# Optimization experiments

Hardware: AMD Instinct MI355X
Metric: run time of the kernel (lower is better)

Reference implementation:

```python
import jax, jax.numpy as jnp
import numpy as np

N, F, HD, E, K, T, IDX = 50000, 128, 256, 800000, 3, 7, 0


def setup_inputs() -> dict:
    key = jax.random.key(0)
    ks = jax.random.split(key, 18)
    s = 0.05  # param init scale
    return {
        "x": jax.random.normal(ks[0], (N, F), jnp.float32),
        "edge_index": jax.random.randint(ks[1], (2, E), 0, N),
        "edge_weight": jax.random.uniform(ks[2], (E,), jnp.float32),
        "h": jax.random.normal(ks[3], (N, HD), jnp.float32),
        "c": jax.random.normal(ks[4], (N, HD), jnp.float32),
        # 4 ChebConvs on X and 4 on H (gates i, f, c, o), each with K Chebyshev weights
        "theta_x": jax.random.normal(ks[5], (4, K, F, HD), jnp.float32) * s,
        "bias_x": jnp.zeros((4, HD), jnp.float32),
        "theta_h": jax.random.normal(ks[6], (4, K, HD, HD), jnp.float32) * s,
        "bias_h": jnp.zeros((4, HD), jnp.float32),
        "w_c": jax.random.normal(ks[7], (3, HD), jnp.float32) * s,  # peephole w_c_i, w_c_f, w_c_o
        "b_gate": jnp.zeros((4, HD), jnp.float32),  # b_i, b_f, b_c, b_o
        # decoder LSTM (input_size=1, hidden=HD), torch gate order i, f, g, o
        "w_ih": jax.random.normal(ks[8], (4 * HD, 1), jnp.float32) * s,
        "w_hh": jax.random.normal(ks[9], (4 * HD, HD), jnp.float32) * s,
        "b_ih": jnp.zeros((4 * HD,), jnp.float32),
        "b_hh": jnp.zeros((4 * HD,), jnp.float32),
        "w_out": jax.random.normal(ks[10], (1, HD), jnp.float32) * s,
        "b_out": jnp.zeros((1,), jnp.float32),
    }


def _cheb_stack(feat, src, dst, w_norm):
    """Stacked Chebyshev bases [K, N, d]; L_hat = -A_norm (sym norm, lambda_max=2)."""
    def lhat(v):
        msg = w_norm[:, None] * v[src]              # [E, d] gather
        return -jax.ops.segment_sum(msg, dst, num_segments=N)  # scatter-add
    Tx = [feat]
    if K > 1:
        Tx.append(lhat(feat))
    for _ in range(2, K):
        Tx.append(2.0 * lhat(Tx[-1]) - Tx[-2])
    return jnp.stack(Tx)


def reference(x, edge_index, edge_weight, h, c, theta_x, bias_x, theta_h, bias_h,
              w_c, b_gate, w_ih, w_hh, b_ih, b_hh, w_out, b_out):
    src, dst = edge_index[0], edge_index[1]
    # ChebConv.__norm__: remove self loops, sym-normalized Laplacian, scale by 2/lambda_max=1,
    # add -I -> L_hat off-diag = -w_norm, diag = 0
    w = jnp.where(src == dst, 0.0, edge_weight)
    deg = jax.ops.segment_sum(w, src, num_segments=N)
    dis = jnp.where(deg > 0, jax.lax.rsqrt(jnp.maximum(deg, 1e-20)), 0.0)
    w_norm = dis[src] * w * dis[dst]

    # GConvLSTM encode: one conv per gate on X and on H; bases shared across gates
    gx = jnp.einsum('knf,gkfo->gno', _cheb_stack(x, src, dst, w_norm), theta_x) + bias_x[:, None, :]
    gh = jnp.einsum('knf,gkfo->gno', _cheb_stack(h, src, dst, w_norm), theta_h) + bias_h[:, None, :]
    g = gx + gh  # [4, N, HD] gates i, f, c, o
    I = jax.nn.sigmoid(g[0] + w_c[0] * c + b_gate[0])
    Fg = jax.nn.sigmoid(g[1] + w_c[1] * c + b_gate[1])
    Cn = Fg * c + I * jnp.tanh(g[2] + b_gate[2])
    O = jax.nn.sigmoid(g[3] + w_c[2] * Cn + b_gate[3])
    Hn = O * jnp.tanh(Cn)

    h0 = Hn[IDX:IDX + 1]          # [1, HD]
    c0 = Cn[IDX:IDX + 1]
    inp0 = x[IDX, -1:][None]      # [1, 1]

    def step(carry, _):
        hd, cd, inp = carry
        gates = inp @ w_ih.T + hd @ w_hh.T + b_ih + b_hh  # [1, 4*HD]
        i, f, gg, o = jnp.split(gates, 4, axis=1)
        cn = jax.nn.sigmoid(f) * cd + jax.nn.sigmoid(i) * jnp.tanh(gg)
        hn = jax.nn.sigmoid(o) * jnp.tanh(cn)
        out = hn @ w_out.T + b_out                         # [1, 1]
        return (hn, cn, out), out

    _, outs = jax.lax.scan(step, (h0, c0, inp0), None, length=T)  # [T, 1, 1]
    prediction = outs[:, :, 0]  # squeeze dim 2 -> [T, 1]
    return prediction
```

## Files before the change

### kernel.cpp

```cpp
#include <hip/hip_runtime.h>
#include <math.h>

#define NN 50000
#define FD 128
#define HDIM 256
#define NE 800000
#define NBR_CAP 512
#define M_CAP 8192
#define TT 7
#define TPB 256
#define GB 96
#define PSLICE 12
#define GRP 21
#define SB 32
#define SPIN_CAP 50000000

#define O_NBRCNT   0
#define O_MCNT     64
#define O_HSYNC    128
#define O_DEG      16512
#define O_BITMAP   216512
#define O_ZERO_END 222784
#define O_NBRNODE  222784
#define O_NBRW     224832
#define O_MS       226880
#define O_MD       259648
#define O_MW       292416
#define O_CF1      325184
#define O_CF2      357952
#define O_GPART    390720

__device__ __forceinline__ float sigm(float v) { return 1.f / (1.f + expf(-v)); }
__device__ __forceinline__ float dis_of(float dg) {
    return dg > 0.f ? rsqrtf(fmaxf(dg, 1e-20f)) : 0.f;
}

__global__ void k_nbr(const int* __restrict__ ei, const float* __restrict__ ew,
                      char* __restrict__ ws) {
    int*   nbrCnt = (int*)(ws + O_NBRCNT);
    int*   nbrNode= (int*)(ws + O_NBRNODE);
    float* nbrW   = (float*)(ws + O_NBRW);

    int gid = blockIdx.x * blockDim.x + threadIdx.x;
    if (gid < (O_ZERO_END - O_MCNT) / 4) ((unsigned*)(ws + O_MCNT))[gid] = 0u;

    int e0 = gid * 4;
    if (e0 >= NE) return;
    int4 d4 = *(const int4*)&ei[NE + e0];
    float4 w4 = *(const float4*)&ew[e0];
    int dd[4] = {d4.x, d4.y, d4.z, d4.w};
    float wv[4] = {w4.x, w4.y, w4.z, w4.w};
    #pragma unroll
    for (int k = 0; k < 4; ++k) {
        if (dd[k] == 0 && wv[k] != 0.f) {
            int s = ei[e0 + k];
            if (s != 0) {
                int slot = atomicAdd(nbrCnt, 1);
                if (slot < NBR_CAP) { nbrNode[slot] = s; nbrW[slot] = wv[k]; }
            }
        }
    }
}

__global__ void k_match(const int* __restrict__ ei, const float* __restrict__ ew,
                        char* __restrict__ ws) {
    const int* nbrCnt = (const int*)(ws + O_NBRCNT);
    const int* nbrNode= (const int*)(ws + O_NBRNODE);
    int*      mCnt   = (int*)(ws + O_MCNT);
    int*      mS     = (int*)(ws + O_MS);
    int*      mD     = (int*)(ws + O_MD);
    float*    mW     = (float*)(ws + O_MW);
    unsigned* bitmap = (unsigned*)(ws + O_BITMAP);

    __shared__ int sNode[NBR_CAP];
    __shared__ int sCnt;
    if (threadIdx.x == 0) sCnt = min(*nbrCnt, NBR_CAP);
    __syncthreads();
    int cnt = sCnt;
    for (int i = threadIdx.x; i < cnt; i += blockDim.x) sNode[i] = nbrNode[i];
    __syncthreads();
    if (blockIdx.x == 0 && threadIdx.x == 0) atomicOr(&bitmap[0], 1u);

    int i = blockIdx.x * blockDim.x + threadIdx.x;
    int e0 = i * 4;
    if (e0 >= NE) return;
    int4 s4 = *(const int4*)&ei[e0];
    int4 d4 = *(const int4*)&ei[NE + e0];
    float4 w4 = *(const float4*)&ew[e0];
    int ss[4] = {s4.x, s4.y, s4.z, s4.w};
    int dd[4] = {d4.x, d4.y, d4.z, d4.w};
    float wv[4] = {w4.x, w4.y, w4.z, w4.w};
    bool m[4];
    #pragma unroll
    for (int k = 0; k < 4; ++k) m[k] = (dd[k] == 0);
    for (int j = 0; j < cnt; ++j) {
        int nv = sNode[j];
        #pragma unroll
        for (int k = 0; k < 4; ++k) m[k] |= (dd[k] == nv);
    }
    #pragma unroll
    for (int k = 0; k < 4; ++k) {
        int s = ss[k], d = dd[k];
        float w = wv[k];
        if (s == d || w == 0.f || !m[k]) continue;
        int slot = atomicAdd(mCnt, 1);
        if (slot < M_CAP) { mS[slot] = s; mD[slot] = d; mW[slot] = w; }
        atomicOr(&bitmap[s >> 5], 1u << (s & 31));
        atomicOr(&bitmap[d >> 5], 1u << (d & 31));
    }
}

__global__ void k_deg(const int* __restrict__ ei, const float* __restrict__ ew,
                      char* __restrict__ ws) {
    const unsigned* bitmap = (const unsigned*)(ws + O_BITMAP);
    float* deg = (float*)(ws + O_DEG);
    int i = blockIdx.x * blockDim.x + threadIdx.x;
    int e0 = i * 4;
    if (e0 >= NE) return;
    int4 s4 = *(const int4*)&ei[e0];
    int4 d4 = *(const int4*)&ei[NE + e0];
    float4 w4 = *(const float4*)&ew[e0];
    int ss[4] = {s4.x, s4.y, s4.z, s4.w};
    int dd[4] = {d4.x, d4.y, d4.z, d4.w};
    float wv[4] = {w4.x, w4.y, w4.z, w4.w};
    #pragma unroll
    for (int k = 0; k < 4; ++k) {
        int s = ss[k];
        if (s == dd[k] || wv[k] == 0.f) continue;
        if (bitmap[s >> 5] & (1u << (s & 31)))
            atomicAdd(&deg[s], wv[k]);
    }
}

__global__ void k_coef(char* __restrict__ ws) {
    const float* deg    = (const float*)(ws + O_DEG);
    const int*   nbrCnt = (const int*)(ws + O_NBRCNT);
    const int*   mCnt   = (const int*)(ws + O_MCNT);
    const int*   nbrNode= (const int*)(ws + O_NBRNODE);
    const float* nbrW   = (const float*)(ws + O_NBRW);
    const int*   mS     = (const int*)(ws + O_MS);
    const int*   mD     = (const int*)(ws + O_MD);
    const float* mW     = (const float*)(ws + O_MW);
    float*       cf1    = (float*)(ws + O_CF1);
    float*       cf2    = (float*)(ws + O_CF2);

    __shared__ int sNode[NBR_CAP];
    __shared__ float sWl[NBR_CAP];
    __shared__ int sCnt, sMcnt;
    const int tid = threadIdx.x;
    if (tid == 0) { sCnt = min(*nbrCnt, NBR_CAP); sMcnt = min(*mCnt, M_CAP); }
    __syncthreads();
    const int ncnt = sCnt, mcnt = sMcnt;
    for (int i = tid; i < ncnt; i += TPB) { sNode[i] = nbrNode[i]; sWl[i] = nbrW[i]; }
    __syncthreads();
    const float dis0 = dis_of(deg[0]);
    for (int i = tid; i < mcnt; i += TPB) {
        int sI = mS[i], dI = mD[i];
        float w = mW[i];
        float disd = dis_of(deg[dI]);
        float wn = dis_of(deg[sI]) * w * disd;
        float Wd = 0.f;
        for (int j = 0; j < ncnt; ++j) Wd += (sNode[j] == dI) ? sWl[j] : 0.f;
        cf1[i] = (dI == 0) ? wn : 0.f;
        cf2[i] = wn * (dis0 * disd * Wd);
    }
}

__global__ __launch_bounds__(TPB) void k_graph(
    const float* __restrict__ x, const float* __restrict__ h,
    const float* __restrict__ theta_x, const float* __restrict__ theta_h,
    char* __restrict__ ws) {

    const int*   mCnt = (const int*)(ws + O_MCNT);
    const int*   mS   = (const int*)(ws + O_MS);
    const float* cf1  = (const float*)(ws + O_CF1);
    const float* cf2  = (const float*)(ws + O_CF2);
    float*       gpart= (float*)(ws + O_GPART);

    __shared__ float tp1[GRP][PSLICE], tp2[GRP][PSLICE];
    __shared__ float tslice[PSLICE];
    __shared__ int   sMcnt;

    const int tid = threadIdx.x, bid = blockIdx.x;
    if (tid == 0) sMcnt = min(*mCnt, M_CAP);
    __syncthreads();
    const int mcnt = sMcnt;

    const bool isx = bid < 32;
    const int qstart = bid * PSLICE - (isx ? 0 : 3 * FD);
    const float* fb0 = isx ? x : h;
    const int fstride = isx ? FD : HDIM;

    const int pl = tid % PSLICE, gr = tid / PSLICE;
    const float* fbase = fb0 + (qstart + pl) % fstride;

    float a1 = 0.f, a2 = 0.f;
    if (gr < GRP) {
        int i = gr;
        for (; i + 3 * GRP < mcnt; i += 4 * GRP) {
            int s0 = mS[i], s1 = mS[i + GRP], s2 = mS[i + 2 * GRP], s3 = mS[i + 3 * GRP];
            float c10 = cf1[i], c11 = cf1[i + GRP], c12 = cf1[i + 2 * GRP], c13 = cf1[i + 3 * GRP];
            float c20 = cf2[i], c21 = cf2[i + GRP], c22 = cf2[i + 2 * GRP], c23 = cf2[i + 3 * GRP];
            float v0 = fbase[(size_t)s0 * fstride];
            float v1 = fbase[(size_t)s1 * fstride];
            float v2 = fbase[(size_t)s2 * fstride];
            float v3 = fbase[(size_t)s3 * fstride];
            a1 += c10 * v0 + c11 * v1 + c12 * v2 + c13 * v3;
            a2 += c20 * v0 + c21 * v1 + c22 * v2 + c23 * v3;
        }
        for (; i < mcnt; i += GRP) {
            float v = fbase[(size_t)mS[i] * fstride];
            a1 += cf1[i] * v;
            a2 += cf2[i] * v;
        }
        tp1[gr][pl] = a1; tp2[gr][pl] = a2;
    }
    __syncthreads();
    if (tid < PSLICE) {
        float A1 = 0.f, A2 = 0.f;
        #pragma unroll
        for (int g2 = 0; g2 < GRP; ++g2) { A1 += tp1[g2][tid]; A2 += tp2[g2][tid]; }
        int q = qstart + tid;
        int ko = q / fstride;
        float ff0 = fb0[q % fstride];
        tslice[tid] = (ko == 0) ? ff0 : ((ko == 1) ? -A1 : 2.f * A2 - ff0);
    }
    __syncthreads();

    {
        const float* tb = isx ? theta_x : theta_h;
        const size_t gs = isx ? (size_t)(3 * FD) * HDIM : (size_t)(3 * HDIM) * HDIM;
        float g0 = 0.f, g1 = 0.f, g2v = 0.f, g3 = 0.f;
        #pragma unroll
        for (int pp = 0; pp < PSLICE; ++pp) {
            float tv = tslice[pp];
            const float* row = tb + (size_t)(qstart + pp) * HDIM;
            g0  += tv * row[tid];
            g1  += tv * row[gs + tid];
            g2v += tv * row[2 * gs + tid];
            g3  += tv * row[3 * gs + tid];
        }
        float* gp = gpart + (size_t)bid * 1024;
        gp[tid] = g0;
        gp[HDIM + tid] = g1;
        gp[2 * HDIM + tid] = g2v;
        gp[3 * HDIM + tid] = g3;
    }
}

__global__ __launch_bounds__(TPB) void k_tail2(
    const float* __restrict__ x, const float* __restrict__ c,
    const float* __restrict__ bias_x, const float* __restrict__ bias_h,
    const float* __restrict__ w_c, const float* __restrict__ b_gate,
    const float* __restrict__ w_ih, const float* __restrict__ w_hh,
    const float* __restrict__ b_ih, const float* __restrict__ b_hh,
    const float* __restrict__ w_out, const float* __restrict__ b_out,
    float* __restrict__ out, char* __restrict__ ws) {

    unsigned long long* hsync = (unsigned long long*)(ws + O_HSYNC);
    const float* gpart = (const float*)(ws + O_GPART);

    __shared__ __align__(16) float sh[HDIM];
    __shared__ float sdot[32];
    __shared__ float swsum[4];

    const int tid = threadIdx.x, bid = blockIdx.x;

    const int rl = tid >> 3, seg = tid & 7;
    const int grow = (rl >> 3) * HDIM + bid * 8 + (rl & 7);
    float4 wreg[8];
    #pragma unroll
    for (int k = 0; k < 8; ++k)
        wreg[k] = *(const float4*)&w_hh[(size_t)grow * HDIM + seg * 32 + k * 4];
    const float wih_r = w_ih[grow];
    const float br    = b_ih[grow] + b_hh[grow];
    const float bo    = b_out[0];
    const float wout_r = w_out[tid];

    {
        const int d = tid >> 3, j = tid & 7;
        const int g = d >> 3, kk = d & 7, o = bid * 8 + kk;
        float s = 0.f;
        #pragma unroll
        for (int pb = j; pb < GB; pb += 8) s += gpart[(size_t)pb * 1024 + g * HDIM + o];
        s += __shfl_down(s, 4);
        s += __shfl_down(s, 2);
        s += __shfl_down(s, 1);
        if (j == 0) sdot[d] = s;
    }
    __syncthreads();

    float creg = 0.f;
    if (tid < 8) {
        const int o = bid * 8 + tid;
        float g0 = sdot[tid]      + bias_x[o]            + bias_h[o];
        float g1 = sdot[8 + tid]  + bias_x[HDIM + o]     + bias_h[HDIM + o];
        float g2 = sdot[16 + tid] + bias_x[2 * HDIM + o] + bias_h[2 * HDIM + o];
        float g3 = sdot[24 + tid] + bias_x[3 * HDIM + o] + bias_h[3 * HDIM + o];
        float c0 = c[o];
        float I  = sigm(g0 + w_c[o] * c0 + b_gate[o]);
        float Fg = sigm(g1 + w_c[HDIM + o] * c0 + b_gate[HDIM + o]);
        float Cn = Fg * c0 + I * tanhf(g2 + b_gate[2 * HDIM + o]);
        float O  = sigm(g3 + w_c[2 * HDIM + o] * Cn + b_gate[3 * HDIM + o]);
        float h0 = O * tanhf(Cn);
        creg = Cn;
        unsigned long long pk = (1ull << 32) | (unsigned long long)__float_as_uint(h0);
        __hip_atomic_store(&hsync[o], pk, __ATOMIC_RELAXED, __HIP_MEMORY_SCOPE_SYSTEM);
    }
    if (tid < 64) {
        #pragma unroll
        for (int j = 0; j < 4; ++j) {
            unsigned long long v;
            int sp = 0;
            do {
                v = __hip_atomic_load(&hsync[tid * 4 + j],
                                      __ATOMIC_RELAXED, __HIP_MEMORY_SCOPE_SYSTEM);
                if ((unsigned)(v >> 32) == 1u) break;
                __builtin_amdgcn_s_sleep(1);
            } while (++sp < SPIN_CAP);
            sh[tid * 4 + j] = __uint_as_float((unsigned)v);
        }
    }
    __syncthreads();
    float sinp = x[FD - 1];

    for (int t = 0; t < TT; ++t) {
        float acc = 0.f;
        const float* shh = &sh[seg * 32];
        #pragma unroll
        for (int k = 0; k < 8; ++k) {
            float4 hv = *(const float4*)&shh[k * 4];
            acc += hv.x * wreg[k].x + hv.y * wreg[k].y + hv.z * wreg[k].z + hv.w * wreg[k].w;
        }
        acc += __shfl_down(acc, 4);
        acc += __shfl_down(acc, 2);
        acc += __shfl_down(acc, 1);
        if (seg == 0) sdot[rl] = acc + sinp * wih_r + br;
        __syncthreads();
        if (tid < 8) {
            float iv = sdot[tid], fv = sdot[8 + tid], gv = sdot[16 + tid], ov = sdot[24 + tid];
            float cn = sigm(fv) * creg + sigm(iv) * tanhf(gv);
            float hn = sigm(ov) * tanhf(cn);
            creg = cn;
            unsigned long long pk = (((unsigned long long)(t + 2)) << 32)
                                  | (unsigned long long)__float_as_uint(hn);
            __hip_atomic_store(&hsync[(t + 1) * HDIM + bid * 8 + tid], pk,
                               __ATOMIC_RELAXED, __HIP_MEMORY_SCOPE_SYSTEM);
        }
        if (tid < 64) {
            #pragma unroll
            for (int j = 0; j < 4; ++j) {
                unsigned long long v;
                int sp = 0;
                do {
                    v = __hip_atomic_load(&hsync[(t + 1) * HDIM + tid * 4 + j],
                                          __ATOMIC_RELAXED, __HIP_MEMORY_SCOPE_SYSTEM);
                    if ((unsigned)(v >> 32) == (unsigned)(t + 2)) break;
                    __builtin_amdgcn_s_sleep(1);
                } while (++sp < SPIN_CAP);
                sh[tid * 4 + j] = __uint_as_float((unsigned)v);
            }
        }
        __syncthreads();
        float pw = wout_r * sh[tid];
        pw += __shfl_down(pw, 32);
        pw += __shfl_down(pw, 16);
        pw += __shfl_down(pw, 8);
        pw += __shfl_down(pw, 4);
        pw += __shfl_down(pw, 2);
        pw += __shfl_down(pw, 1);
        if ((tid & 63) == 0) swsum[tid >> 6] = pw;
        __syncthreads();
        float sval = swsum[0] + swsum[1] + swsum[2] + swsum[3] + bo;
        sinp = sval;
        if (bid == 0 && tid == 0) out[t] = sval;
    }
}

extern "C" void kernel_launch(void* const* d_in, const int* in_sizes, int n_in,
                              void* d_out, int out_size, void* d_ws, size_t ws_size,
                              hipStream_t stream) {
    const float* x       = (const float*)d_in[0];
    const int*   ei      = (const int*)d_in[1];
    const float* ew      = (const float*)d_in[2];
    const float* h       = (const float*)d_in[3];
    const float* c       = (const float*)d_in[4];
    const float* theta_x = (const float*)d_in[5];
    const float* bias_x  = (const float*)d_in[6];
    const float* theta_h = (const float*)d_in[7];
    const float* bias_h  = (const float*)d_in[8];
    const float* w_c     = (const float*)d_in[9];
    const float* b_gate  = (const float*)d_in[10];
    const float* w_ih    = (const float*)d_in[11];
    const float* w_hh    = (const float*)d_in[12];
    const float* b_ih    = (const float*)d_in[13];
    const float* b_hh    = (const float*)d_in[14];
    const float* w_out   = (const float*)d_in[15];
    const float* b_out   = (const float*)d_in[16];
    char* ws = (char*)d_ws;
    float* out = (float*)d_out;

    hipMemsetAsync(ws, 0, 64, stream);

    int eb4 = (NE / 4 + TPB - 1) / TPB;
    k_nbr<<<eb4, TPB, 0, stream>>>(ei, ew, ws);
    k_match<<<eb4, TPB, 0, stream>>>(ei, ew, ws);
    k_deg<<<eb4, TPB, 0, stream>>>(ei, ew, ws);
    k_coef<<<1, TPB, 0, stream>>>(ws);
    k_graph<<<GB, TPB, 0, stream>>>(x, h, theta_x, theta_h, ws);
    k_tail2<<<SB, TPB, 0, stream>>>(x, c, bias_x, bias_h, w_c, b_gate,
                                    w_ih, w_hh, b_ih, b_hh, w_out, b_out, out, ws);
}
```

Before: 58.51 us.

## Fuse coefficient computation into graph kernel and widen spin-wait polling

Removes the single-block k_coef kernel and recomputes the per-edge Chebyshev coefficients redundantly inside each k_graph block, staging them chunk by chunk in shared memory. This drops one kernel launch and a serial single-block stage, at the cost of every one of the 96 blocks repeating the coefficient work, including the neighbour-scan loop. Separately, in the LSTM tail every thread now polls one hsync entry without s_sleep, instead of 64 threads polling four entries each. The per-step shared-memory barrier before the output reduction is also removed.

```diff
diff --git a/kernel.cpp b/kernel.cpp
--- a/kernel.cpp
+++ b/kernel.cpp
@@ -12,6 +12,7 @@
 #define GB 96
 #define PSLICE 12
 #define GRP 21
+#define ECHUNK 2048
 #define SB 32
 #define SPIN_CAP 50000000
 
@@ -26,9 +27,7 @@
 #define O_MS       226880
 #define O_MD       259648
 #define O_MW       292416
-#define O_CF1      325184
-#define O_CF2      357952
-#define O_GPART    390720
+#define O_GPART    325184
 
 __device__ __forceinline__ float sigm(float v) { return 1.f / (1.f + expf(-v)); }
 __device__ __forceinline__ float dis_of(float dg) {
@@ -132,7 +131,11 @@
     }
 }
 
-__global__ void k_coef(char* __restrict__ ws) {
+__global__ __launch_bounds__(TPB) void k_graph(
+    const float* __restrict__ x, const float* __restrict__ h,
+    const float* __restrict__ theta_x, const float* __restrict__ theta_h,
+    char* __restrict__ ws) {
+
     const float* deg    = (const float*)(ws + O_DEG);
     const int*   nbrCnt = (const int*)(ws + O_NBRCNT);
     const int*   mCnt   = (const int*)(ws + O_MCNT);
@@ -141,50 +144,22 @@
     const int*   mS     = (const int*)(ws + O_MS);
     const int*   mD     = (const int*)(ws + O_MD);
     const float* mW     = (const float*)(ws + O_MW);
-    float*       cf1    = (float*)(ws + O_CF1);
-    float*       cf2    = (float*)(ws + O_CF2);
-
-    __shared__ int sNode[NBR_CAP];
+    float*       gpart  = (float*)(ws + O_GPART);
+
+    __shared__ int   sNode[NBR_CAP];
     __shared__ float sWl[NBR_CAP];
-    __shared__ int sCnt, sMcnt;
-    const int tid = threadIdx.x;
+    __shared__ float cf1[ECHUNK], cf2[ECHUNK];
+    __shared__ int   sS[ECHUNK];
+    __shared__ float tp1[GRP][PSLICE], tp2[GRP][PSLICE];
+    __shared__ float tslice[PSLICE];
+    __shared__ int   sCnt, sMcnt;
+
+    const int tid = threadIdx.x, bid = blockIdx.x;
     if (tid == 0) { sCnt = min(*nbrCnt, NBR_CAP); sMcnt = min(*mCnt, M_CAP); }
     __syncthreads();
     const int ncnt = sCnt, mcnt = sMcnt;
     for (int i = tid; i < ncnt; i += TPB) { sNode[i] = nbrNode[i]; sWl[i] = nbrW[i]; }
     __syncthreads();
-    const float dis0 = dis_of(deg[0]);
-    for (int i = tid; i < mcnt; i += TPB) {
-        int sI = mS[i], dI = mD[i];
-        float w = mW[i];
-        float disd = dis_of(deg[dI]);
-        float wn = dis_of(deg[sI]) * w * disd;
-        float Wd = 0.f;
-        for (int j = 0; j < ncnt; ++j) Wd += (sNode[j] == dI) ? sWl[j] : 0.f;
-        cf1[i] = (dI == 0) ? wn : 0.f;
-        cf2[i] = wn * (dis0 * disd * Wd);
-    }
-}
-
-__global__ __launch_bounds__(TPB) void k_graph(
-    const float* __restrict__ x, const float* __restrict__ h,
-    const float* __restrict__ theta_x, const float* __restrict__ theta_h,
-    char* __restrict__ ws) {
-
-    const int*   mCnt = (const int*)(ws + O_MCNT);
-    const int*   mS   = (const int*)(ws + O_MS);
-    const float* cf1  = (const float*)(ws + O_CF1);
-    const float* cf2  = (const float*)(ws + O_CF2);
-    float*       gpart= (float*)(ws + O_GPART);
-
-    __shared__ float tp1[GRP][PSLICE], tp2[GRP][PSLICE];
-    __shared__ float tslice[PSLICE];
-    __shared__ int   sMcnt;
-
-    const int tid = threadIdx.x, bid = blockIdx.x;
-    if (tid == 0) sMcnt = min(*mCnt, M_CAP);
-    __syncthreads();
-    const int mcnt = sMcnt;
 
     const bool isx = bid < 32;
     const int qstart = bid * PSLICE - (isx ? 0 : 3 * FD);
@@ -193,28 +168,45 @@
 
     const int pl = tid % PSLICE, gr = tid / PSLICE;
     const float* fbase = fb0 + (qstart + pl) % fstride;
+    const float dis0 = dis_of(deg[0]);
 
     float a1 = 0.f, a2 = 0.f;
-    if (gr < GRP) {
-        int i = gr;
-        for (; i + 3 * GRP < mcnt; i += 4 * GRP) {
-            int s0 = mS[i], s1 = mS[i + GRP], s2 = mS[i + 2 * GRP], s3 = mS[i + 3 * GRP];
-            float c10 = cf1[i], c11 = cf1[i + GRP], c12 = cf1[i + 2 * GRP], c13 = cf1[i + 3 * GRP];
-            float c20 = cf2[i], c21 = cf2[i + GRP], c22 = cf2[i + 2 * GRP], c23 = cf2[i + 3 * GRP];
-            float v0 = fbase[(size_t)s0 * fstride];
-            float v1 = fbase[(size_t)s1 * fstride];
-            float v2 = fbase[(size_t)s2 * fstride];
-            float v3 = fbase[(size_t)s3 * fstride];
-            a1 += c10 * v0 + c11 * v1 + c12 * v2 + c13 * v3;
-            a2 += c20 * v0 + c21 * v1 + c22 * v2 + c23 * v3;
-        }
-        for (; i < mcnt; i += GRP) {
-            float v = fbase[(size_t)mS[i] * fstride];
-            a1 += cf1[i] * v;
-            a2 += cf2[i] * v;
-        }
-        tp1[gr][pl] = a1; tp2[gr][pl] = a2;
-    }
+    for (int c0i = 0; c0i < mcnt; c0i += ECHUNK) {
+        int clen = min(ECHUNK, mcnt - c0i);
+        for (int i = tid; i < clen; i += TPB) {
+            int sI = mS[c0i + i], dI = mD[c0i + i];
+            float w = mW[c0i + i];
+            float disd = dis_of(deg[dI]);
+            float wn = dis_of(deg[sI]) * w * disd;
+            float Wd = 0.f;
+            for (int j = 0; j < ncnt; ++j) Wd += (sNode[j] == dI) ? sWl[j] : 0.f;
+            cf1[i] = (dI == 0) ? wn : 0.f;
+            cf2[i] = wn * (dis0 * disd * Wd);
+            sS[i] = sI;
+        }
+        __syncthreads();
+        if (gr < GRP) {
+            int i = gr;
+            for (; i + 3 * GRP < clen; i += 4 * GRP) {
+                int s0 = sS[i], s1 = sS[i + GRP], s2 = sS[i + 2 * GRP], s3 = sS[i + 3 * GRP];
+                float c10 = cf1[i], c11 = cf1[i + GRP], c12 = cf1[i + 2 * GRP], c13 = cf1[i + 3 * GRP];
+                float c20 = cf2[i], c21 = cf2[i + GRP], c22 = cf2[i + 2 * GRP], c23 = cf2[i + 3 * GRP];
+                float v0 = fbase[(size_t)s0 * fstride];
+                float v1 = fbase[(size_t)s1 * fstride];
+                float v2 = fbase[(size_t)s2 * fstride];
+                float v3 = fbase[(size_t)s3 * fstride];
+                a1 += c10 * v0 + c11 * v1 + c12 * v2 + c13 * v3;
+                a2 += c20 * v0 + c21 * v1 + c22 * v2 + c23 * v3;
+            }
+            for (; i < clen; i += GRP) {
+                float v = fbase[(size_t)sS[i] * fstride];
+                a1 += cf1[i] * v;
+                a2 += cf2[i] * v;
+            }
+        }
+        __syncthreads();
+    }
+    if (gr < GRP) { tp1[gr][pl] = a1; tp2[gr][pl] = a2; }
     __syncthreads();
     if (tid < PSLICE) {
         float A1 = 0.f, A2 = 0.f;
@@ -307,19 +299,14 @@
         unsigned long long pk = (1ull << 32) | (unsigned long long)__float_as_uint(h0);
         __hip_atomic_store(&hsync[o], pk, __ATOMIC_RELAXED, __HIP_MEMORY_SCOPE_SYSTEM);
     }
-    if (tid < 64) {
-        #pragma unroll
-        for (int j = 0; j < 4; ++j) {
-            unsigned long long v;
-            int sp = 0;
-            do {
-                v = __hip_atomic_load(&hsync[tid * 4 + j],
-                                      __ATOMIC_RELAXED, __HIP_MEMORY_SCOPE_SYSTEM);
-                if ((unsigned)(v >> 32) == 1u) break;
-                __builtin_amdgcn_s_sleep(1);
-            } while (++sp < SPIN_CAP);
-            sh[tid * 4 + j] = __uint_as_float((unsigned)v);
-        }
+    {
+        unsigned long long v;
+        int sp = 0;
+        do {
+            v = __hip_atomic_load(&hsync[tid], __ATOMIC_RELAXED, __HIP_MEMORY_SCOPE_SYSTEM);
+            if ((unsigned)(v >> 32) == 1u) break;
+        } while (++sp < SPIN_CAP);
+        sh[tid] = __uint_as_float((unsigned)v);
     }
     __syncthreads();
     float sinp = x[FD - 1];
@@ -347,22 +334,19 @@
             __hip_atomic_store(&hsync[(t + 1) * HDIM + bid * 8 + tid], pk,
                                __ATOMIC_RELAXED, __HIP_MEMORY_SCOPE_SYSTEM);
         }
-        if (tid < 64) {
-            #pragma unroll
-            for (int j = 0; j < 4; ++j) {
-                unsigned long long v;
-                int sp = 0;
-                do {
-                    v = __hip_atomic_load(&hsync[(t + 1) * HDIM + tid * 4 + j],
-                                          __ATOMIC_RELAXED, __HIP_MEMORY_SCOPE_SYSTEM);
-                    if ((unsigned)(v >> 32) == (unsigned)(t + 2)) break;
-                    __builtin_amdgcn_s_sleep(1);
-                } while (++sp < SPIN_CAP);
-                sh[tid * 4 + j] = __uint_as_float((unsigned)v);
-            }
-        }
-        __syncthreads();
-        float pw = wout_r * sh[tid];
+        float hval;
+        {
+            unsigned long long v;
+            int sp = 0;
+            do {
+                v = __hip_atomic_load(&hsync[(t + 1) * HDIM + tid],
+                                      __ATOMIC_RELAXED, __HIP_MEMORY_SCOPE_SYSTEM);
+                if ((unsigned)(v >> 32) == (unsigned)(t + 2)) break;
+            } while (++sp < SPIN_CAP);
+            hval = __uint_as_float((unsigned)v);
+        }
+        sh[tid] = hval;
+        float pw = wout_r * hval;
         pw += __shfl_down(pw, 32);
         pw += __shfl_down(pw, 16);
         pw += __shfl_down(pw, 8);
@@ -406,7 +390,6 @@
     k_nbr<<<eb4, TPB, 0, stream>>>(ei, ew, ws);
     k_match<<<eb4, TPB, 0, stream>>>(ei, ew, ws);
     k_deg<<<eb4, TPB, 0, stream>>>(ei, ew, ws);
-    k_coef<<<1, TPB, 0, stream>>>(ws);
     k_graph<<<GB, TPB, 0, stream>>>(x, h, theta_x, theta_h, ws);
     k_tail2<<<SB, TPB, 0, stream>>>(x, c, bias_x, bias_h, w_c, b_gate,
                                     w_ih, w_hh, b_ih, b_hh, w_out, b_out, out, ws);
```

Result: faster. 52.87 us, median of 2 (-9.6%).
